# Optimization experiments

Hardware: AMD Instinct MI355X
Metric: run time of the kernel (lower is better)

Reference implementation:

```python
import jax, jax.numpy as jnp
import numpy as np
from jax import lax

M_DIM = 128
L1 = L2 = L3 = L4 = 4
L = L1 * L2 * L3 * L4  # 256
RANK = 2
BATCH, D = 4, 16
W = D - RANK + 1  # 15 windows per dim (linear mode, stride 1, drop)


def _make_bbasis():
    # Bbasis[idx, i] = prod_d cos(2*pi*(j_d+1)/(i+2)), idx = ((j1*L2+j2)*L3+j3)*L4+j4
    i = jnp.arange(M_DIM, dtype=jnp.float32)
    def c(Ld):
        j = jnp.arange(D_ := Ld, dtype=jnp.float32)
        return jnp.cos(2.0 * jnp.pi * (j[:, None] + 1.0) / (i[None, :] + 2.0))  # (Ld, m)
    B1, B2, B3, B4 = c(L1), c(L2), c(L3), c(L4)
    Bb = (B1[:, None, None, None, :] * B2[None, :, None, None, :]
          * B3[None, None, :, None, :] * B4[None, None, None, :, :])
    return Bb.reshape(L, M_DIM).astype(jnp.float32)


def setup_inputs() -> dict:
    key = jax.random.key(0)
    k1, k2, k3 = jax.random.split(key, 3)
    vec_arr = jax.random.normal(k1, (BATCH, D, D, D, D, M_DIM), dtype=jnp.float32)
    # M initialized as identity + small noise (nn.init.eye_ is exactly eye; noise keeps grads non-trivial)
    M = jnp.eye(M_DIM, dtype=jnp.float32) + 0.01 * jax.random.normal(k2, (M_DIM, M_DIM), dtype=jnp.float32)
    Acoeff = jax.random.uniform(k3, (M_DIM, L), minval=-0.1, maxval=0.1, dtype=jnp.float32)
    Bbasis = _make_bbasis()
    return {"vec_arr": vec_arr, "M": M, "Acoeff": Acoeff, "Bbasis": Bbasis}


def _basis_index():
    # window coords k_d in [0, W), basis index uses j_d = k_d mod L_d
    k = jnp.arange(W)
    j1 = (k % L1)[:, None, None, None]
    j2 = (k % L2)[None, :, None, None]
    j3 = (k % L3)[None, None, :, None]
    j4 = (k % L4)[None, None, None, :]
    idx = ((j1 * L2 + j2) * L3 + j3) * L4 + j4  # (W,W,W,W)
    return idx.reshape(-1)  # (W^4,)


def reference(vec_arr, M, Acoeff, Bbasis):
    # 4D sliding-window mean (linear mode, stride 1, 'drop'), rank_op='avg'.
    # mean(window @ M.T) == mean(window) @ M.T (linearity), so pool then one GEMM.
    win = (1, RANK, RANK, RANK, RANK, 1)
    pooled = lax.reduce_window(vec_arr, jnp.float32(0.0), lax.add, win,
                               (1, 1, 1, 1, 1, 1), 'VALID') / float(RANK ** 4)
    # agg[b, k1..k4, j] = sum_i pooled[...,i] * M[j,i]  (i.e. x @ M.T)
    agg = jnp.einsum('bwxyzi,ji->bwxyzj', pooled, M)  # (B, W,W,W,W, m)
    agg = agg.reshape(agg.shape[0], -1, M_DIM)        # (B, W^4, m)
    idx = _basis_index()                               # (W^4,)
    # Position-dependent descriptor N(k) = Acoeff[:, idx] * Bbasis[idx, :]
    Nk = Acoeff.T[idx] * Bbasis[idx]                   # (W^4, m)
    return Nk[None, :, :] - agg                        # (B, W^4, m) deviation
```

## Files before the change

### kernel.cpp

```cpp
#include <hip/hip_runtime.h>
#include <hip/hip_bf16.h>
#include <stdint.h>

#define MD   128
#define LBAS 256

#define MBF_OFF 131072ull
#define WS_NEED (131072ull + 32768ull)

typedef __attribute__((ext_vector_type(8))) __bf16 bf16x8;
typedef __attribute__((ext_vector_type(4))) float floatx4;
typedef __attribute__((ext_vector_type(8))) unsigned short ushortx8;
typedef __attribute__((ext_vector_type(4))) unsigned short ushortx4;

__device__ __forceinline__ float bf2f(unsigned short u){
  union { unsigned int i; float f; } v; v.i = ((unsigned int)u) << 16; return v.f;
}
__device__ __forceinline__ unsigned short f2bf(float x){
  union { float f; unsigned int i; } v; v.f = x;
  unsigned int r = v.i + 0x7FFFu + ((v.i >> 16) & 1u);
  return (unsigned short)(r >> 16);
}
__device__ __forceinline__ int detect_f32(const void* Bbasis){
  return ((const unsigned int*)Bbasis)[0] == 0x3F800000u;
}

__global__ __launch_bounds__(256) void nk2_kernel(const void* __restrict__ Acoeff,
                                                  const void* __restrict__ Bbasis,
                                                  const void* __restrict__ Mmat,
                                                  float* __restrict__ NkFull,
                                                  unsigned short* __restrict__ Mbf){
  int gid = blockIdx.x * 256 + threadIdx.x;
  const int isf = detect_f32(Bbasis);
  if (gid < LBAS * MD){
    int idx = gid >> 7, j = gid & 127;
    float a, b;
    if (isf){ a = ((const float*)Acoeff)[j*LBAS+idx]; b = ((const float*)Bbasis)[idx*MD+j]; }
    else    { a = bf2f(((const unsigned short*)Acoeff)[j*LBAS+idx]);
              b = bf2f(((const unsigned short*)Bbasis)[idx*MD+j]); }
    NkFull[gid] = a * b;
  } else {
    int m = gid - LBAS * MD;
    if (m < MD * MD){
      Mbf[m] = isf ? f2bf(((const float*)Mmat)[m]) : ((const unsigned short*)Mmat)[m];
    }
  }
}

__global__ __launch_bounds__(256, 4) void mega_kernel(const void* __restrict__ vec,
                                                      const float* __restrict__ NkFull,
                                                      const unsigned short* __restrict__ Mbf,
                                                      const void* __restrict__ Bbasis,
                                                      void* __restrict__ out){
  __shared__ __align__(16) float S[32 * 132];
  __shared__ __align__(16) unsigned short Ab[16 * 136];
  __shared__ __align__(16) float sNk[16 * 128];

  const int xcd  = blockIdx.x & 7;
  const int slot = blockIdx.x >> 3;
  const int b    = xcd >> 1;
  const int s    = slot * 2 + (xcd & 1);
  if (s >= 225) return;
  const int w3 = s / 15;
  const int w2 = s - w3 * 15;
  const int t  = threadIdx.x;
  const int isf = detect_f32(Bbasis);

  const int wave = t >> 6, lane = t & 63;
  const int quad = lane >> 4, l16 = lane & 15;

  const size_t vbase0 = (size_t)b * 8388608 + (size_t)w2 * 32768 + (size_t)w3 * 2048;

  int offF[4];
#pragma unroll
  for (int k = 0; k < 4; ++k){
    const int ci = k * 256 + t;
    const int row = ci >> 5;
    offF[k] = (row >> 4) * 2048 + (row & 15) * 128 + (ci & 31) * 4;
  }
  int offB[2];
#pragma unroll
  for (int k = 0; k < 2; ++k){
    const int ci = k * 256 + t;
    const int row = ci >> 4;
    offB[k] = (row >> 4) * 2048 + (row & 15) * 128 + (ci & 15) * 8;
  }

  floatx4 pre[4][2];

  if (isf){
    const float* vf = (const float*)vec + vbase0;
#pragma unroll
    for (int k = 0; k < 4; ++k){
      pre[k][0] = *(const floatx4*)(vf + offF[k]);
      pre[k][1] = *(const floatx4*)(vf + offF[k] + 32768);
    }
  } else {
    const unsigned short* vh = (const unsigned short*)vec + vbase0;
#pragma unroll
    for (int k = 0; k < 2; ++k){
      *(ushortx8*)&pre[k][0] = *(const ushortx8*)(vh + offB[k]);
      *(ushortx8*)&pre[k][1] = *(const ushortx8*)(vh + offB[k] + 32768);
    }
  }

  bf16x8 mfr[2][4];
#pragma unroll
  for (int cc = 0; cc < 2; ++cc)
#pragma unroll
    for (int s4 = 0; s4 < 4; ++s4)
      *(ushortx8*)&mfr[cc][s4] =
          *(const ushortx8*)(Mbf + ((wave * 2 + cc) * 16 + l16) * 128 + s4 * 32 + quad * 8);

  {
    const int j2f = (w2 & 3), j3f = (w3 & 3);
#pragma unroll
    for (int k = 0; k < 2; ++k){
      const int ci = k * 256 + t;
      const int row16 = ci >> 5, c4 = (ci & 31) * 4;
      const int j1 = row16 >> 2, j4 = row16 & 3;
      const int nkrow = ((j1 * 4 + j2f) * 4 + j3f) * 4 + j4;
      *(floatx4*)&sNk[row16 * 128 + c4] = *(const floatx4*)&NkFull[nkrow * 128 + c4];
    }
  }

  const int pw4 = t >> 4;
  const int pc8 = (t & 15) * 8;
  const int owner = (t < 240);
  float prv[8];

  for (int x1 = 0; x1 < 16; ++x1){
    __syncthreads();

    if (isf){
#pragma unroll
      for (int k = 0; k < 4; ++k){
        const int ci = k * 256 + t;
        const int row = ci >> 5, c4 = (ci & 31) * 4;
        floatx4 sv;
#pragma unroll
        for (int q = 0; q < 4; ++q) sv[q] = pre[k][0][q] + pre[k][1][q];
        *(floatx4*)&S[row * 132 + c4] = sv;
      }
    } else {
#pragma unroll
      for (int k = 0; k < 2; ++k){
        const int ci = k * 256 + t;
        const int row = ci >> 4, c8 = (ci & 15) * 8;
        const ushortx8 a = *(const ushortx8*)&pre[k][0];
        const ushortx8 c = *(const ushortx8*)&pre[k][1];
#pragma unroll
        for (int q = 0; q < 8; ++q) S[row * 132 + c8 + q] = bf2f(a[q]) + bf2f(c[q]);
      }
    }

    if (x1 < 15){
      if (isf){
        const float* vf = (const float*)vec + vbase0 + (size_t)(x1 + 1) * 524288;
#pragma unroll
        for (int k = 0; k < 4; ++k){
          pre[k][0] = *(const floatx4*)(vf + offF[k]);
          pre[k][1] = *(const floatx4*)(vf + offF[k] + 32768);
        }
      } else {
        const unsigned short* vh = (const unsigned short*)vec + vbase0 + (size_t)(x1 + 1) * 524288;
#pragma unroll
        for (int k = 0; k < 2; ++k){
          *(ushortx8*)&pre[k][0] = *(const ushortx8*)(vh + offB[k]);
          *(ushortx8*)&pre[k][1] = *(const ushortx8*)(vh + offB[k] + 32768);
        }
      }
    }
    __syncthreads();

    if (owner){
      float cur[8];
      const int p0 = pw4 * 132 + pc8;
#pragma unroll
      for (int e = 0; e < 8; ++e)
        cur[e] = ((S[p0 + e] + S[p0 + 132 + e]) +
                  (S[p0 + 16 * 132 + e] + S[p0 + 17 * 132 + e])) * 0.125f;
      if (x1 > 0){
        ushortx8 av;
#pragma unroll
        for (int e = 0; e < 8; ++e) av[e] = f2bf((cur[e] + prv[e]) * 0.5f);
        *(ushortx8*)&Ab[pw4 * 136 + pc8] = av;
      }
#pragma unroll
      for (int e = 0; e < 8; ++e) prv[e] = cur[e];
    }
    __syncthreads();

    if (x1 > 0){
      floatx4 acc[2];
      acc[0] = (floatx4){0.f,0.f,0.f,0.f};
      acc[1] = (floatx4){0.f,0.f,0.f,0.f};
#pragma unroll
      for (int s4 = 0; s4 < 4; ++s4){
        const bf16x8 af = *(const bf16x8*)&Ab[l16 * 136 + s4 * 32 + quad * 8];
#pragma unroll
        for (int cc = 0; cc < 2; ++cc){
          acc[cc] = __builtin_amdgcn_mfma_f32_16x16x32_bf16(af, mfr[cc][s4], acc[cc], 0, 0, 0);
        }
      }

      const int j1sel = (x1 - 1) & 3;
      const size_t outBase = ((size_t)(((b * 15 + (x1 - 1)) * 15 + w2) * 15 + w3)) * 15;
      const int col0 = wave * 32 + l16;
#pragma unroll
      for (int cc = 0; cc < 2; ++cc){
        const int col = col0 + cc * 16;
#pragma unroll
        for (int reg = 0; reg < 4; ++reg){
          const int row = quad * 4 + reg;
          if (row < 15){
            const float nk = sNk[(j1sel * 4 + (row & 3)) * 128 + col];
            const float o = nk - acc[cc][reg];
            if (isf){
              ((float*)out)[(outBase + row) * 128 + col] = o;
            } else {
              ((unsigned short*)out)[(outBase + row) * 128 + col] = f2bf(o);
            }
          }
        }
      }
    }
  }
}

extern "C" void kernel_launch(void* const* d_in, const int* in_sizes, int n_in,
                              void* d_out, int out_size, void* d_ws, size_t ws_size,
                              hipStream_t stream) {
  const void* vec = d_in[0];
  const void* Mm  = d_in[1];
  const void* Ac  = d_in[2];
  const void* Bb  = d_in[3];

  float* NkFull = (float*)d_ws;
  unsigned short* Mbf = (unsigned short*)((char*)d_ws + MBF_OFF);

  nk2_kernel<<<192, 256, 0, stream>>>(Ac, Bb, Mm, NkFull, Mbf);
  mega_kernel<<<904, 256, 0, stream>>>(vec, NkFull, Mbf, Bb, d_out);
}
```

Baseline: 261.7 us.

## Split x1 loop across two blocks and stage MFMA output through LDS for vector stores

Each (b,w2,w3) column is now split into two halves along x1 (0..8 and 8..15), doubling the grid to 1800 blocks, with one overlapping slice recomputed per half. MFMA accumulators are written to a shared tile and re-read so that output is stored as coalesced 16-byte vectors rather than scattered scalar stores. The pooling reads from shared memory are vectorised, and the next-slice prefetch is moved after the MFMA. The cost is an extra barrier per step, more shared memory per block, and one redundant input slice per half.

```diff
diff --git a/kernel.cpp b/kernel.cpp
--- a/kernel.cpp
+++ b/kernel.cpp
@@ -53,19 +53,24 @@
                                                       const void* __restrict__ Bbasis,
                                                       void* __restrict__ out){
   __shared__ __align__(16) float S[32 * 132];
+  __shared__ __align__(16) float Ct[16 * 132];
   __shared__ __align__(16) unsigned short Ab[16 * 136];
   __shared__ __align__(16) float sNk[16 * 128];
 
   const int xcd  = blockIdx.x & 7;
   const int slot = blockIdx.x >> 3;
   const int b    = xcd >> 1;
-  const int s    = slot * 2 + (xcd & 1);
-  if (s >= 225) return;
+  const int u    = slot * 2 + (xcd & 1);
+  const int s    = u >> 1;
+  const int h    = u & 1;
   const int w3 = s / 15;
   const int w2 = s - w3 * 15;
   const int t  = threadIdx.x;
   const int isf = detect_f32(Bbasis);
 
+  const int x1beg = h ? 8 : 0;
+  const int x1end = h ? 16 : 9;
+
   const int wave = t >> 6, lane = t & 63;
   const int quad = lane >> 4, l16 = lane & 15;
 
@@ -89,14 +94,14 @@
   floatx4 pre[4][2];
 
   if (isf){
-    const float* vf = (const float*)vec + vbase0;
+    const float* vf = (const float*)vec + vbase0 + (size_t)x1beg * 524288;
 #pragma unroll
     for (int k = 0; k < 4; ++k){
       pre[k][0] = *(const floatx4*)(vf + offF[k]);
       pre[k][1] = *(const floatx4*)(vf + offF[k] + 32768);
     }
   } else {
-    const unsigned short* vh = (const unsigned short*)vec + vbase0;
+    const unsigned short* vh = (const unsigned short*)vec + vbase0 + (size_t)x1beg * 524288;
 #pragma unroll
     for (int k = 0; k < 2; ++k){
       *(ushortx8*)&pre[k][0] = *(const ushortx8*)(vh + offB[k]);
@@ -129,9 +134,7 @@
   const int owner = (t < 240);
   float prv[8];
 
-  for (int x1 = 0; x1 < 16; ++x1){
-    __syncthreads();
-
+  for (int s1 = x1beg; s1 < x1end; ++s1){
     if (isf){
 #pragma unroll
       for (int k = 0; k < 4; ++k){
@@ -153,34 +156,24 @@
         for (int q = 0; q < 8; ++q) S[row * 132 + c8 + q] = bf2f(a[q]) + bf2f(c[q]);
       }
     }
-
-    if (x1 < 15){
-      if (isf){
-        const float* vf = (const float*)vec + vbase0 + (size_t)(x1 + 1) * 524288;
-#pragma unroll
-        for (int k = 0; k < 4; ++k){
-          pre[k][0] = *(const floatx4*)(vf + offF[k]);
-          pre[k][1] = *(const floatx4*)(vf + offF[k] + 32768);
-        }
-      } else {
-        const unsigned short* vh = (const unsigned short*)vec + vbase0 + (size_t)(x1 + 1) * 524288;
-#pragma unroll
-        for (int k = 0; k < 2; ++k){
-          *(ushortx8*)&pre[k][0] = *(const ushortx8*)(vh + offB[k]);
-          *(ushortx8*)&pre[k][1] = *(const ushortx8*)(vh + offB[k] + 32768);
-        }
-      }
-    }
     __syncthreads();
 
     if (owner){
+      const int p0 = pw4 * 132 + pc8;
+      const floatx4 a0 = *(const floatx4*)&S[p0];
+      const floatx4 a1 = *(const floatx4*)&S[p0 + 4];
+      const floatx4 b0 = *(const floatx4*)&S[p0 + 132];
+      const floatx4 b1 = *(const floatx4*)&S[p0 + 136];
+      const floatx4 c0 = *(const floatx4*)&S[p0 + 16 * 132];
+      const floatx4 c1 = *(const floatx4*)&S[p0 + 16 * 132 + 4];
+      const floatx4 d0 = *(const floatx4*)&S[p0 + 17 * 132];
+      const floatx4 d1 = *(const floatx4*)&S[p0 + 17 * 132 + 4];
       float cur[8];
-      const int p0 = pw4 * 132 + pc8;
-#pragma unroll
-      for (int e = 0; e < 8; ++e)
-        cur[e] = ((S[p0 + e] + S[p0 + 132 + e]) +
-                  (S[p0 + 16 * 132 + e] + S[p0 + 17 * 132 + e])) * 0.125f;
-      if (x1 > 0){
+      const floatx4 lo = ((a0 + b0) + (c0 + d0)) * 0.125f;
+      const floatx4 hi = ((a1 + b1) + (c1 + d1)) * 0.125f;
+#pragma unroll
+      for (int e = 0; e < 4; ++e){ cur[e] = lo[e]; cur[4 + e] = hi[e]; }
+      if (s1 > x1beg){
         ushortx8 av;
 #pragma unroll
         for (int e = 0; e < 8; ++e) av[e] = f2bf((cur[e] + prv[e]) * 0.5f);
@@ -191,7 +184,7 @@
     }
     __syncthreads();
 
-    if (x1 > 0){
+    if (s1 > x1beg){
       floatx4 acc[2];
       acc[0] = (floatx4){0.f,0.f,0.f,0.f};
       acc[1] = (floatx4){0.f,0.f,0.f,0.f};
@@ -203,24 +196,69 @@
           acc[cc] = __builtin_amdgcn_mfma_f32_16x16x32_bf16(af, mfr[cc][s4], acc[cc], 0, 0, 0);
         }
       }
-
-      const int j1sel = (x1 - 1) & 3;
-      const size_t outBase = ((size_t)(((b * 15 + (x1 - 1)) * 15 + w2) * 15 + w3)) * 15;
-      const int col0 = wave * 32 + l16;
-#pragma unroll
-      for (int cc = 0; cc < 2; ++cc){
-        const int col = col0 + cc * 16;
-#pragma unroll
-        for (int reg = 0; reg < 4; ++reg){
-          const int row = quad * 4 + reg;
-          if (row < 15){
-            const float nk = sNk[(j1sel * 4 + (row & 3)) * 128 + col];
-            const float o = nk - acc[cc][reg];
-            if (isf){
-              ((float*)out)[(outBase + row) * 128 + col] = o;
-            } else {
-              ((unsigned short*)out)[(outBase + row) * 128 + col] = f2bf(o);
-            }
+#pragma unroll
+      for (int cc = 0; cc < 2; ++cc)
+#pragma unroll
+        for (int reg = 0; reg < 4; ++reg)
+          Ct[(quad * 4 + reg) * 132 + (wave * 2 + cc) * 16 + l16] = acc[cc][reg];
+      __syncthreads();
+
+      if (s1 + 1 < x1end){
+        if (isf){
+          const float* vf = (const float*)vec + vbase0 + (size_t)(s1 + 1) * 524288;
+#pragma unroll
+          for (int k = 0; k < 4; ++k){
+            pre[k][0] = *(const floatx4*)(vf + offF[k]);
+            pre[k][1] = *(const floatx4*)(vf + offF[k] + 32768);
+          }
+        } else {
+          const unsigned short* vh = (const unsigned short*)vec + vbase0 + (size_t)(s1 + 1) * 524288;
+#pragma unroll
+          for (int k = 0; k < 2; ++k){
+            *(ushortx8*)&pre[k][0] = *(const ushortx8*)(vh + offB[k]);
+            *(ushortx8*)&pre[k][1] = *(const ushortx8*)(vh + offB[k] + 32768);
+          }
+        }
+      }
+
+      const int w1 = s1 - 1;
+      const int j1sel = w1 & 3;
+      const size_t outBase = ((size_t)(((b * 15 + w1) * 15 + w2) * 15 + w3)) * 15;
+#pragma unroll
+      for (int k = 0; k < 2; ++k){
+        const int ci = k * 256 + t;
+        if (ci < 480){
+          const int row = ci >> 5, c4 = (ci & 31) * 4;
+          const floatx4 v  = *(const floatx4*)&Ct[row * 132 + c4];
+          const floatx4 nk = *(const floatx4*)&sNk[(j1sel * 4 + (row & 3)) * 128 + c4];
+          floatx4 o;
+#pragma unroll
+          for (int e = 0; e < 4; ++e) o[e] = nk[e] - v[e];
+          if (isf){
+            *(floatx4*)((float*)out + (outBase + row) * 128 + c4) = o;
+          } else {
+            ushortx4 ob;
+#pragma unroll
+            for (int e = 0; e < 4; ++e) ob[e] = f2bf(o[e]);
+            *(ushortx4*)((unsigned short*)out + (outBase + row) * 128 + c4) = ob;
+          }
+        }
+      }
+    } else {
+      if (s1 + 1 < x1end){
+        if (isf){
+          const float* vf = (const float*)vec + vbase0 + (size_t)(s1 + 1) * 524288;
+#pragma unroll
+          for (int k = 0; k < 4; ++k){
+            pre[k][0] = *(const floatx4*)(vf + offF[k]);
+            pre[k][1] = *(const floatx4*)(vf + offF[k] + 32768);
+          }
+        } else {
+          const unsigned short* vh = (const unsigned short*)vec + vbase0 + (size_t)(s1 + 1) * 524288;
+#pragma unroll
+          for (int k = 0; k < 2; ++k){
+            *(ushortx8*)&pre[k][0] = *(const ushortx8*)(vh + offB[k]);
+            *(ushortx8*)&pre[k][1] = *(const ushortx8*)(vh + offB[k] + 32768);
           }
         }
       }
@@ -240,5 +278,5 @@
   unsigned short* Mbf = (unsigned short*)((char*)d_ws + MBF_OFF);
 
   nk2_kernel<<<192, 256, 0, stream>>>(Ac, Bb, Mm, NkFull, Mbf);
-  mega_kernel<<<904, 256, 0, stream>>>(vec, NkFull, Mbf, Bb, d_out);
-}
+  mega_kernel<<<1800, 256, 0, stream>>>(vec, NkFull, Mbf, Bb, d_out);
+}
```

Result: slower. 271.9 us (+3.9%).
